# Kernel optimization log

Hardware: AMD Instinct MI355X
Metric: run time of the kernel (lower is better)

The kernel has to match this reference:

```python
import jax, jax.numpy as jnp
import numpy as np

T, B, IN_DIM = 512, 256, 256
H1, H = 512, 256          # fc hidden, GRU hidden
OUT_DIM = 18


def setup_inputs() -> dict:
    key = jax.random.key(0)
    ks = jax.random.split(key, 14)
    s = 0.05
    return {
        "x":      jax.random.normal(ks[0], (T, B, IN_DIM), dtype=jnp.float32),
        # fc1: Linear(IN_DIM,H1)+ReLU, Linear(H1,H)+ReLU
        "W_fc1a": jax.random.normal(ks[1], (H1, IN_DIM), dtype=jnp.float32) * s,
        "b_fc1a": jax.random.normal(ks[2], (H1,), dtype=jnp.float32) * s,
        "W_fc1b": jax.random.normal(ks[3], (H, H1), dtype=jnp.float32) * s,
        "b_fc1b": jax.random.normal(ks[4], (H,), dtype=jnp.float32) * s,
        # GRUCell(H, H): weights ordered [r, z, n] like torch
        "W_ih":   jax.random.normal(ks[5], (3 * H, H), dtype=jnp.float32) * s,
        "b_ih":   jax.random.normal(ks[6], (3 * H,), dtype=jnp.float32) * s,
        "W_hh":   jax.random.normal(ks[7], (3 * H, H), dtype=jnp.float32) * s,
        "b_hh":   jax.random.normal(ks[8], (3 * H,), dtype=jnp.float32) * s,
        # fc2: Linear(H,H1)+ReLU, Linear(H1,OUT_DIM)
        "W_fc2a": jax.random.normal(ks[9], (H1, H), dtype=jnp.float32) * s,
        "b_fc2a": jax.random.normal(ks[10], (H1,), dtype=jnp.float32) * s,
        "W_fc2b": jax.random.normal(ks[11], (OUT_DIM, H1), dtype=jnp.float32) * s,
        "b_fc2b": jax.random.normal(ks[12], (OUT_DIM,), dtype=jnp.float32) * s,
    }


def reference(x, W_fc1a, b_fc1a, W_fc1b, b_fc1b,
              W_ih, b_ih, W_hh, b_hh,
              W_fc2a, b_fc2a, W_fc2b, b_fc2b):
    batch = x.shape[1]
    h0 = jnp.zeros((batch, W_hh.shape[1]), dtype=x.dtype)

    def step(h, xt):
        # fc1 MLP
        a = jax.nn.relu(xt @ W_fc1a.T + b_fc1a)
        a = jax.nn.relu(a @ W_fc1b.T + b_fc1b)
        # GRUCell (torch gate order r, z, n)
        gi = a @ W_ih.T + b_ih            # [B, 3H]
        gh = h @ W_hh.T + b_hh            # [B, 3H]
        i_r, i_z, i_n = jnp.split(gi, 3, axis=-1)
        h_r, h_z, h_n = jnp.split(gh, 3, axis=-1)
        r = jax.nn.sigmoid(i_r + h_r)
        z = jax.nn.sigmoid(i_z + h_z)
        n = jnp.tanh(i_n + r * h_n)
        h_new = (1.0 - z) * n + z * h
        # fc2 head
        q = jax.nn.relu(h_new @ W_fc2a.T + b_fc2a) @ W_fc2b.T + b_fc2b
        return h_new, q

    _, qs = jax.lax.scan(step, h0, x)     # qs: [T, B, OUT_DIM]
    return qs
```

## Files before the change

kernel.cpp:

```cpp
#include <hip/hip_runtime.h>
#include <hip/hip_fp16.h>
#include <cstdio>

typedef unsigned short u16;
typedef __attribute__((ext_vector_type(8))) _Float16 f16x8;
typedef __attribute__((ext_vector_type(4))) float fv4;

#define TT 512
#define BB 256

__device__ __forceinline__ float us2f(u16 u) {
    union { u16 u; _Float16 h; } c; c.u = u; return (float)c.h;
}
__device__ __forceinline__ u16 f2us(float f) {
    union { u16 u; _Float16 h; } c; c.h = (_Float16)f; return c.u;
}

__device__ __forceinline__ void gl_lds16(const u16* g, u16* l) {
    __builtin_amdgcn_global_load_lds(
        (const __attribute__((address_space(1))) void*)g,
        (__attribute__((address_space(3))) void*)l, 16, 0, 0);
}

__device__ __forceinline__ void sync_lds() {
    __builtin_amdgcn_s_waitcnt(0xC00F);
    __builtin_amdgcn_s_barrier();
}

__global__ void cvt_f32_f16(const float* __restrict__ s, u16* __restrict__ d, int n) {
    long stride = (long)gridDim.x * blockDim.x * 8;
    for (long i = ((long)blockIdx.x * blockDim.x + threadIdx.x) * 8; i < n; i += stride) {
        f16x8 o;
#pragma unroll
        for (int j = 0; j < 8; ++j) o[j] = (_Float16)s[i + j];
        *(f16x8*)(d + i) = o;
    }
}

__global__ void bias_fold(const float* __restrict__ bih, const float* __restrict__ bhh,
                          float* __restrict__ bsum) {
    int i = blockIdx.x * blockDim.x + threadIdx.x;
    if (i < 768) bsum[i] = bih[i] + (i < 512 ? bhh[i] : 0.f);
}

__global__ void pack_whh(const float* __restrict__ W, u16* __restrict__ Wp) {
    int t = blockIdx.x * blockDim.x + threadIdx.x;
    int l = t & 63;
    int kt = (t >> 6) & 7;
    int jt = t >> 9;
    int j = jt * 16 + (l & 15);
    int k = kt * 32 + (l >> 4) * 8;
    f16x8 o;
#pragma unroll
    for (int i = 0; i < 8; ++i) o[i] = (_Float16)W[j * 256 + k + i];
    *(f16x8*)(Wp + (size_t)t * 8) = o;
}

__global__ void pack_w2b(const float* __restrict__ W, u16* __restrict__ Wp) {
    int t = blockIdx.x * blockDim.x + threadIdx.x;
    int l = t & 63;
    int kt = (t >> 6) & 15;
    int nt = t >> 10;
    int n = nt * 16 + (l & 15);
    int k = kt * 32 + (l >> 4) * 8;
    f16x8 o;
#pragma unroll
    for (int i = 0; i < 8; ++i)
        o[i] = (n < 18) ? (_Float16)W[n * 512 + k + i] : (_Float16)0.f;
    *(f16x8*)(Wp + (size_t)t * 8) = o;
}

__global__ __launch_bounds__(256) void gemm_bt(
    const u16* __restrict__ A, const u16* __restrict__ B,
    const float* __restrict__ bias, u16* __restrict__ C,
    int N, int K, int act)
{
    __shared__ u16 Ash[4096] __attribute__((aligned(16)));
    __shared__ u16 Bsh[4096] __attribute__((aligned(16)));
    const int tid = threadIdx.x;
    const int l = tid & 63, w = tid >> 6;
    const long m0 = (long)blockIdx.y * 128;
    const int n0 = blockIdx.x * 128;
    const int r = tid >> 2, c8 = (tid & 3) * 8;
    const u16* gA0 = A + (m0 + r) * K + c8;
    const u16* gA1 = A + (m0 + 64 + r) * K + c8;
    const u16* gB0 = B + (long)(n0 + r) * K + c8;
    const u16* gB1 = B + (long)(n0 + 64 + r) * K + c8;
    const int mb = (w >> 1) * 64, nb = (w & 1) * 64;
    const int mrow = l & 15, colq = (l >> 4) * 8;
    fv4 acc[4][4] = {};
    for (int k0 = 0; k0 < K; k0 += 32) {
        gl_lds16(gA0 + k0, &Ash[tid * 8]);
        gl_lds16(gA1 + k0, &Ash[2048 + tid * 8]);
        gl_lds16(gB0 + k0, &Bsh[tid * 8]);
        gl_lds16(gB1 + k0, &Bsh[2048 + tid * 8]);
        __syncthreads();
        f16x8 af[4], bf[4];
#pragma unroll
        for (int i = 0; i < 4; ++i)
            af[i] = *(const f16x8*)&Ash[(mb + i * 16 + mrow) * 32 + colq];
#pragma unroll
        for (int i = 0; i < 4; ++i)
            bf[i] = *(const f16x8*)&Bsh[(nb + i * 16 + mrow) * 32 + colq];
#pragma unroll
        for (int mt = 0; mt < 4; ++mt)
#pragma unroll
            for (int nt = 0; nt < 4; ++nt)
                acc[mt][nt] = __builtin_amdgcn_mfma_f32_16x16x32_f16(
                    af[mt], bf[nt], acc[mt][nt], 0, 0, 0);
        __syncthreads();
    }
    float bv[4];
#pragma unroll
    for (int nt = 0; nt < 4; ++nt) bv[nt] = bias[n0 + nb + nt * 16 + mrow];
    const int rq = (l >> 4) * 4;
#pragma unroll
    for (int mt = 0; mt < 4; ++mt)
#pragma unroll
        for (int nt = 0; nt < 4; ++nt)
#pragma unroll
            for (int i = 0; i < 4; ++i) {
                float v = acc[mt][nt][i] + bv[nt];
                if (act) v = fmaxf(v, 0.f);
                C[(m0 + mb + mt * 16 + rq + i) * (long)N + (n0 + nb + nt * 16 + mrow)] = f2us(v);
            }
}

__global__ __launch_bounds__(256) void gemm_gi(
    const u16* __restrict__ A, const u16* __restrict__ B,
    const float* __restrict__ bias, u16* __restrict__ GIp)
{
    __shared__ u16 Ash[4096] __attribute__((aligned(16)));
    __shared__ u16 Bsh[4096] __attribute__((aligned(16)));
    const int tid = threadIdx.x;
    const int l = tid & 63, w = tid >> 6;
    const long m0 = (long)blockIdx.y * 128;
    const int n0 = blockIdx.x * 128;
    const int r = tid >> 2, c8 = (tid & 3) * 8;
    const u16* gA0 = A + (m0 + r) * 256 + c8;
    const u16* gA1 = A + (m0 + 64 + r) * 256 + c8;
    const u16* gB0 = B + (long)(n0 + r) * 256 + c8;
    const u16* gB1 = B + (long)(n0 + 64 + r) * 256 + c8;
    const int mb = (w >> 1) * 64, nb = (w & 1) * 64;
    const int mrow = l & 15, colq = (l >> 4) * 8;
    fv4 acc[4][4] = {};
    for (int k0 = 0; k0 < 256; k0 += 32) {
        gl_lds16(gA0 + k0, &Ash[tid * 8]);
        gl_lds16(gA1 + k0, &Ash[2048 + tid * 8]);
        gl_lds16(gB0 + k0, &Bsh[tid * 8]);
        gl_lds16(gB1 + k0, &Bsh[2048 + tid * 8]);
        __syncthreads();
        f16x8 af[4], bf[4];
#pragma unroll
        for (int i = 0; i < 4; ++i)
            af[i] = *(const f16x8*)&Ash[(mb + i * 16 + mrow) * 32 + colq];
#pragma unroll
        for (int i = 0; i < 4; ++i)
            bf[i] = *(const f16x8*)&Bsh[(nb + i * 16 + mrow) * 32 + colq];
#pragma unroll
        for (int mt = 0; mt < 4; ++mt)
#pragma unroll
            for (int nt = 0; nt < 4; ++nt)
                acc[mt][nt] = __builtin_amdgcn_mfma_f32_16x16x32_f16(
                    af[mt], bf[nt], acc[mt][nt], 0, 0, 0);
        __syncthreads();
    }
    float bv[4];
#pragma unroll
    for (int nt = 0; nt < 4; ++nt) bv[nt] = bias[n0 + nb + nt * 16 + mrow];
    const int rq = (l >> 4) * 4;
#pragma unroll
    for (int mt = 0; mt < 4; ++mt)
#pragma unroll
        for (int nt = 0; nt < 4; ++nt)
#pragma unroll
            for (int i = 0; i < 4; ++i) {
                float v = acc[mt][nt][i] + bv[nt];
                int m = (int)(m0 + mb + mt * 16 + rq + i);
                int n = n0 + nb + nt * 16 + mrow;
                int t  = m >> 8, b = m & 255;
                int blk = b >> 4, rb = b & 15, q = rb >> 2, i2 = rb & 3;
                int g = n >> 8, c = n & 255, w2 = c >> 5, s = (c >> 4) & 1, cl = c & 15;
                size_t idx = ((((size_t)t * 16 + blk) * 8 + w2) * 64 + (q * 16 + cl)) * 24
                             + (g * 2 + s) * 4 + i2;
                GIp[idx] = f2us(v);
            }
}

__global__ __launch_bounds__(512)
__attribute__((amdgpu_waves_per_eu(2, 2)))
void gru_seq5(u16* Wp, const u16* __restrict__ GIp,
              const float* __restrict__ bhh, u16* Hout)
{
    __shared__ u16 h_sh[4096] __attribute__((aligned(16)));
    __shared__ u16 Wl[24576] __attribute__((aligned(16)));
    const int tid = threadIdx.x;
    const int l = tid & 63, w = tid >> 6;
    const int blk = blockIdx.x;
    const int bg = blk * 16;
    const int col = l & 15, quad = l >> 4;

    for (int i = tid; i < 4096; i += 512) h_sh[i] = 0;
    for (int idx = tid; idx < 3072; idx += 512)
        *(f16x8*)&Wl[(size_t)idx * 8] =
            *(const f16x8*)&Wp[(((size_t)(idx >> 6) * 8 + 7) * 64 + (idx & 63)) * 8];

    int jts[6];
#pragma unroll
    for (int g = 0; g < 3; ++g)
#pragma unroll
        for (int s = 0; s < 2; ++s) jts[g * 2 + s] = g * 16 + 2 * w + s;

    f16x8 wf[6][7];
#pragma unroll
    for (int u = 0; u < 6; ++u)
#pragma unroll
        for (int kt = 0; kt < 7; ++kt)
            wf[u][kt] = *(const f16x8*)&Wp[(((size_t)jts[u] * 8 + kt) * 64 + l) * 8];

    float hbn[2] = { bhh[512 + 32 * w + col], bhh[512 + 32 * w + 16 + col] };

    const u16* gbase = GIp + ((size_t)(blk * 8 + w) * 64 + l) * 24;
    float hold[2][4] = {};
    u16* hout_base = Hout + ((size_t)(bg + quad * 4) * 256) + 32 * w + col;
    __syncthreads();

    for (int t = 0; t < TT; ++t) {
        const u16* gp = gbase + (size_t)t * 196608;
        f16x8 gcur[3];
#pragma unroll
        for (int j = 0; j < 3; ++j) gcur[j] = *(const f16x8*)(gp + j * 8);

        fv4 acc[6] = {};
#pragma unroll
        for (int kt = 0; kt < 7; ++kt) {
            f16x8 a = *(const f16x8*)&h_sh[(kt * 64 + l) * 8];
#pragma unroll
            for (int u = 0; u < 6; ++u)
                acc[u] = __builtin_amdgcn_mfma_f32_16x16x32_f16(a, wf[u][kt], acc[u], 0, 0, 0);
        }
        {
            f16x8 a = *(const f16x8*)&h_sh[(7 * 64 + l) * 8];
#pragma unroll
            for (int u = 0; u < 6; ++u) {
                f16x8 bw = *(const f16x8*)&Wl[(size_t)(jts[u] * 64 + l) * 8];
                acc[u] = __builtin_amdgcn_mfma_f32_16x16x32_f16(a, bw, acc[u], 0, 0, 0);
            }
        }
        sync_lds();

        u16* hp = hout_base + (size_t)t * 65536;
#pragma unroll
        for (int s = 0; s < 2; ++s) {
            const int q2 = s * 2 + (col >> 3);
#pragma unroll
            for (int i = 0; i < 4; ++i) {
                float pr  = (float)gcur[0][s * 4 + i] + acc[0 + s][i];
                float pz  = (float)gcur[1][s * 4 + i] + acc[2 + s][i];
                float h_n = acc[4 + s][i] + hbn[s];
                float rg = __builtin_amdgcn_rcpf(1.f + __expf(-pr));
                float zg = __builtin_amdgcn_rcpf(1.f + __expf(-pz));
                float pre = (float)gcur[2][s * 4 + i] + rg * h_n;
                float ea = __expf(-2.f * fabsf(pre));
                float th = (1.f - ea) * __builtin_amdgcn_rcpf(1.f + ea);
                float ng = (pre >= 0.f) ? th : -th;
                float hn = (1.f - zg) * ng + zg * hold[s][i];
                hold[s][i] = hn;
                u16 hu = f2us(hn);
                h_sh[(w * 64 + q2 * 16 + quad * 4 + i) * 8 + (col & 7)] = hu;
                hp[(size_t)i * 256 + s * 16] = hu;
            }
        }
        sync_lds();
    }
}

__global__ __launch_bounds__(256) void head_gemm(
    const u16* __restrict__ Q1, const u16* __restrict__ W2p,
    const float* __restrict__ b2, float* __restrict__ out)
{
    __shared__ u16 Ash[4096] __attribute__((aligned(16)));
    __shared__ u16 Bsh[16384] __attribute__((aligned(16)));
    const int tid = threadIdx.x;
    const int l = tid & 63, w = tid >> 6;
    const long m0 = (long)blockIdx.x * 128;
    const int col = l & 15, quad = l >> 4, colq = quad * 8;
    for (int i = tid * 8; i < 16384; i += 2048)
        *(f16x8*)&Bsh[i] = *(const f16x8*)&W2p[i];
    const int r = tid >> 2, c8 = (tid & 3) * 8;
    const u16* gA0 = Q1 + (m0 + r) * 512 + c8;
    const u16* gA1 = Q1 + (m0 + 64 + r) * 512 + c8;
    fv4 acc[2][2] = {};
    for (int k0 = 0; k0 < 512; k0 += 32) {
        gl_lds16(gA0 + k0, &Ash[tid * 8]);
        gl_lds16(gA1 + k0, &Ash[2048 + tid * 8]);
        __syncthreads();
        const int kt = k0 >> 5;
        f16x8 af[2], bf[2];
#pragma unroll
        for (int mt = 0; mt < 2; ++mt)
            af[mt] = *(const f16x8*)&Ash[(w * 32 + mt * 16 + col) * 32 + colq];
#pragma unroll
        for (int nt = 0; nt < 2; ++nt)
            bf[nt] = *(const f16x8*)&Bsh[((nt * 16 + kt) * 64 + l) * 8];
#pragma unroll
        for (int mt = 0; mt < 2; ++mt)
#pragma unroll
            for (int nt = 0; nt < 2; ++nt)
                acc[mt][nt] = __builtin_amdgcn_mfma_f32_16x16x32_f16(
                    af[mt], bf[nt], acc[mt][nt], 0, 0, 0);
        __syncthreads();
    }
    const int rq = quad * 4;
#pragma unroll
    for (int nt = 0; nt < 2; ++nt) {
        int c = nt * 16 + col;
        if (c < 18) {
            float bias = b2[c];
#pragma unroll
            for (int mt = 0; mt < 2; ++mt)
#pragma unroll
                for (int i = 0; i < 4; ++i)
                    out[(m0 + w * 32 + mt * 16 + rq + i) * 18 + c] = acc[mt][nt][i] + bias;
        }
    }
}

extern "C" void kernel_launch(void* const* d_in, const int* in_sizes, int n_in,
                              void* d_out, int out_size, void* d_ws, size_t ws_size,
                              hipStream_t stream) {
    const float* x   = (const float*)d_in[0];
    const float* W1a = (const float*)d_in[1];
    const float* b1a = (const float*)d_in[2];
    const float* W1b = (const float*)d_in[3];
    const float* b1b = (const float*)d_in[4];
    const float* Wih = (const float*)d_in[5];
    const float* bih = (const float*)d_in[6];
    const float* Whh = (const float*)d_in[7];
    const float* bhh = (const float*)d_in[8];
    const float* W2a = (const float*)d_in[9];
    const float* b2a = (const float*)d_in[10];
    const float* W2b = (const float*)d_in[11];
    const float* b2b = (const float*)d_in[12];

    char* ws = (char*)d_ws;
    u16* R    = (u16*)ws;
    u16* A2b  = (u16*)(ws + 201326592);
    u16* XH   = (u16*)(ws + 268435456);
    float* bsum = (float*)(ws + 268435456 + 67108864 - 4096);
    u16* W1ah = (u16*)(ws + 335544320);
    u16* W1bh = (u16*)(ws + 335806464);
    u16* Wihh = (u16*)(ws + 336068608);
    u16* W2ah = (u16*)(ws + 336461824);
    u16* Wpk  = (u16*)(ws + 336723968);
    u16* W2p  = (u16*)(ws + 337117184);
    if (ws_size < 337149952) {
        fprintf(stderr, "kernel_launch: ws too small (%zu < 337149952)\n", ws_size);
    }

    cvt_f32_f16<<<dim3(2048), dim3(256), 0, stream>>>(x, XH, 33554432);
    cvt_f32_f16<<<dim3(64), dim3(256), 0, stream>>>(W1a, W1ah, 131072);
    cvt_f32_f16<<<dim3(64), dim3(256), 0, stream>>>(W1b, W1bh, 131072);
    cvt_f32_f16<<<dim3(96), dim3(256), 0, stream>>>(Wih, Wihh, 196608);
    cvt_f32_f16<<<dim3(64), dim3(256), 0, stream>>>(W2a, W2ah, 131072);
    pack_whh<<<dim3(96), dim3(256), 0, stream>>>(Whh, Wpk);
    pack_w2b<<<dim3(8), dim3(256), 0, stream>>>(W2b, W2p);

    gemm_bt<<<dim3(4, 1024), dim3(256), 0, stream>>>(XH, W1ah, b1a, R,   512, 256, 1);
    bias_fold<<<dim3(3), dim3(256), 0, stream>>>(bih, bhh, bsum);
    gemm_bt<<<dim3(2, 1024), dim3(256), 0, stream>>>(R,  W1bh, b1b, A2b, 256, 512, 1);
    gemm_gi<<<dim3(6, 1024), dim3(256), 0, stream>>>(A2b, Wihh, bsum, R);
    gru_seq5<<<dim3(16), dim3(512), 0, stream>>>(Wpk, R, bhh, XH);
    gemm_bt<<<dim3(4, 1024), dim3(256), 0, stream>>>(XH, W2ah, b2a, R, 512, 256, 1);
    head_gemm<<<dim3(1024), dim3(256), 0, stream>>>(R, W2p, b2b, (float*)d_out);
}
```

Before: 1.568 ms.

## Halve GRU waves per block and double-buffer hidden state to drop a barrier

The recurrent GRU kernel now runs 4 waves of 256 threads instead of 8. Each wave computes 12 gate tiles instead of 6, keeping twice as many W_hh fragments in registers. The hidden state in LDS is double-buffered, which removes the barrier between the MFMA reads and the h writes and leaves one sync per timestep. The GI layout written by gemm_gi is re-packed to match, with 48 halves per lane. The cost is much higher register pressure (84 f16x8 weight fragments per lane at 1 wave/EU) and less parallelism per step, which risks spills.

```diff
diff --git a/kernel.cpp b/kernel.cpp
--- a/kernel.cpp
+++ b/kernel.cpp
@@ -180,19 +180,20 @@
                 int n = n0 + nb + nt * 16 + mrow;
                 int t  = m >> 8, b = m & 255;
                 int blk = b >> 4, rb = b & 15, q = rb >> 2, i2 = rb & 3;
-                int g = n >> 8, c = n & 255, w2 = c >> 5, s = (c >> 4) & 1, cl = c & 15;
-                size_t idx = ((((size_t)t * 16 + blk) * 8 + w2) * 64 + (q * 16 + cl)) * 24
-                             + (g * 2 + s) * 4 + i2;
+                int g = n >> 8, c = n & 255;
+                int w2 = c >> 6, s = (c >> 4) & 3, cl = c & 15;
+                size_t idx = ((((size_t)t * 16 + blk) * 4 + w2) * 64 + (q * 16 + cl)) * 48
+                             + (size_t)(g * 16 + s * 4 + i2);
                 GIp[idx] = f2us(v);
             }
 }
 
-__global__ __launch_bounds__(512)
-__attribute__((amdgpu_waves_per_eu(2, 2)))
-void gru_seq5(u16* Wp, const u16* __restrict__ GIp,
+__global__ __attribute__((amdgpu_flat_work_group_size(256, 256)))
+__attribute__((amdgpu_waves_per_eu(1, 1)))
+void gru_seq6(u16* Wp, const u16* __restrict__ GIp,
               const float* __restrict__ bhh, u16* Hout)
 {
-    __shared__ u16 h_sh[4096] __attribute__((aligned(16)));
+    __shared__ u16 h_sh[2][4096] __attribute__((aligned(16)));
     __shared__ u16 Wl[24576] __attribute__((aligned(16)));
     const int tid = threadIdx.x;
     const int l = tid & 63, w = tid >> 6;
@@ -200,74 +201,78 @@
     const int bg = blk * 16;
     const int col = l & 15, quad = l >> 4;
 
-    for (int i = tid; i < 4096; i += 512) h_sh[i] = 0;
-    for (int idx = tid; idx < 3072; idx += 512)
+    for (int i = tid; i < 4096; i += 256) h_sh[0][i] = 0;
+    for (int idx = tid; idx < 3072; idx += 256)
         *(f16x8*)&Wl[(size_t)idx * 8] =
             *(const f16x8*)&Wp[(((size_t)(idx >> 6) * 8 + 7) * 64 + (idx & 63)) * 8];
 
-    int jts[6];
+    int jts[12];
 #pragma unroll
     for (int g = 0; g < 3; ++g)
 #pragma unroll
-        for (int s = 0; s < 2; ++s) jts[g * 2 + s] = g * 16 + 2 * w + s;
-
-    f16x8 wf[6][7];
-#pragma unroll
-    for (int u = 0; u < 6; ++u)
+        for (int s = 0; s < 4; ++s) jts[g * 4 + s] = g * 16 + 4 * w + s;
+
+    f16x8 wf[12][7];
+#pragma unroll
+    for (int u = 0; u < 12; ++u)
 #pragma unroll
         for (int kt = 0; kt < 7; ++kt)
             wf[u][kt] = *(const f16x8*)&Wp[(((size_t)jts[u] * 8 + kt) * 64 + l) * 8];
 
-    float hbn[2] = { bhh[512 + 32 * w + col], bhh[512 + 32 * w + 16 + col] };
-
-    const u16* gbase = GIp + ((size_t)(blk * 8 + w) * 64 + l) * 24;
-    float hold[2][4] = {};
-    u16* hout_base = Hout + ((size_t)(bg + quad * 4) * 256) + 32 * w + col;
+    float hbn[4];
+#pragma unroll
+    for (int s = 0; s < 4; ++s) hbn[s] = bhh[512 + (4 * w + s) * 16 + col];
+
+    const u16* gbase = GIp + ((size_t)(blk * 4 + w) * 64 + l) * 48;
+    float hold[4][4] = {};
+    u16* hout_base = Hout + ((size_t)(bg + quad * 4) * 256) + 4 * w * 16 + col;
     __syncthreads();
 
     for (int t = 0; t < TT; ++t) {
+        const int rd = t & 1, wr = (t + 1) & 1;
         const u16* gp = gbase + (size_t)t * 196608;
-        f16x8 gcur[3];
-#pragma unroll
-        for (int j = 0; j < 3; ++j) gcur[j] = *(const f16x8*)(gp + j * 8);
-
-        fv4 acc[6] = {};
+        f16x8 gcur[6];
+#pragma unroll
+        for (int j = 0; j < 6; ++j) gcur[j] = *(const f16x8*)(gp + j * 8);
+
+        fv4 acc[12] = {};
 #pragma unroll
         for (int kt = 0; kt < 7; ++kt) {
-            f16x8 a = *(const f16x8*)&h_sh[(kt * 64 + l) * 8];
-#pragma unroll
-            for (int u = 0; u < 6; ++u)
+            f16x8 a = *(const f16x8*)&h_sh[rd][(kt * 64 + l) * 8];
+#pragma unroll
+            for (int u = 0; u < 12; ++u)
                 acc[u] = __builtin_amdgcn_mfma_f32_16x16x32_f16(a, wf[u][kt], acc[u], 0, 0, 0);
         }
         {
-            f16x8 a = *(const f16x8*)&h_sh[(7 * 64 + l) * 8];
-#pragma unroll
-            for (int u = 0; u < 6; ++u) {
+            f16x8 a = *(const f16x8*)&h_sh[rd][(7 * 64 + l) * 8];
+#pragma unroll
+            for (int u = 0; u < 12; ++u) {
                 f16x8 bw = *(const f16x8*)&Wl[(size_t)(jts[u] * 64 + l) * 8];
                 acc[u] = __builtin_amdgcn_mfma_f32_16x16x32_f16(a, bw, acc[u], 0, 0, 0);
             }
         }
-        sync_lds();
 
         u16* hp = hout_base + (size_t)t * 65536;
 #pragma unroll
-        for (int s = 0; s < 2; ++s) {
-            const int q2 = s * 2 + (col >> 3);
+        for (int s = 0; s < 4; ++s) {
+            const int q2 = (s & 1) * 2 + (col >> 3);
+            const int ktw = 2 * w + (s >> 1);
 #pragma unroll
             for (int i = 0; i < 4; ++i) {
-                float pr  = (float)gcur[0][s * 4 + i] + acc[0 + s][i];
-                float pz  = (float)gcur[1][s * 4 + i] + acc[2 + s][i];
-                float h_n = acc[4 + s][i] + hbn[s];
+                const int e = s * 4 + i;
+                float pr  = (float)gcur[(e >> 3)][e & 7] + acc[0 + s][i];
+                float pz  = (float)gcur[2 + (e >> 3)][e & 7] + acc[4 + s][i];
+                float h_n = acc[8 + s][i] + hbn[s];
                 float rg = __builtin_amdgcn_rcpf(1.f + __expf(-pr));
                 float zg = __builtin_amdgcn_rcpf(1.f + __expf(-pz));
-                float pre = (float)gcur[2][s * 4 + i] + rg * h_n;
+                float pre = (float)gcur[4 + (e >> 3)][e & 7] + rg * h_n;
                 float ea = __expf(-2.f * fabsf(pre));
                 float th = (1.f - ea) * __builtin_amdgcn_rcpf(1.f + ea);
                 float ng = (pre >= 0.f) ? th : -th;
                 float hn = (1.f - zg) * ng + zg * hold[s][i];
                 hold[s][i] = hn;
                 u16 hu = f2us(hn);
-                h_sh[(w * 64 + q2 * 16 + quad * 4 + i) * 8 + (col & 7)] = hu;
+                h_sh[wr][(ktw * 64 + q2 * 16 + quad * 4 + i) * 8 + (col & 7)] = hu;
                 hp[(size_t)i * 256 + s * 16] = hu;
             }
         }
@@ -370,7 +375,7 @@
     bias_fold<<<dim3(3), dim3(256), 0, stream>>>(bih, bhh, bsum);
     gemm_bt<<<dim3(2, 1024), dim3(256), 0, stream>>>(R,  W1bh, b1b, A2b, 256, 512, 1);
     gemm_gi<<<dim3(6, 1024), dim3(256), 0, stream>>>(A2b, Wihh, bsum, R);
-    gru_seq5<<<dim3(16), dim3(512), 0, stream>>>(Wpk, R, bhh, XH);
+    gru_seq6<<<dim3(16), dim3(256), 0, stream>>>(Wpk, R, bhh, XH);
     gemm_bt<<<dim3(4, 1024), dim3(256), 0, stream>>>(XH, W2ah, b2a, R, 512, 256, 1);
     head_gemm<<<dim3(1024), dim3(256), 0, stream>>>(R, W2p, b2b, (float*)d_out);
 }
```

Measured after the change: 2.341 ms. 49.3% more time.
